# Performance work log

Measured on AMD Instinct MI355X. Metric: run time of the kernel, lower is better.

## Reference

```python
import jax, jax.numpy as jnp
import numpy as np
import math

# Config (mirrors KoopmanConfig)
B = 4096          # batch
C = 128           # context_dim
D = 32            # latent_dim
K = 8             # num_experts
R = 8             # low_rank
NSEG = 3
STEPS = [8, 8, 8] # steps_per_segment, sums to HORIZON
HORIZON = 24
DT = 0.1
DECAY_TARGET = 0.7
DECAY_SCALE = 1.0
SIGMA_MAX = 1.0
MAX_FROB = 3.0
TEMP = 2.0        # gate_temperature_start (stage 1)
EPS = 1e-6


def expm_fixed(M):
    """Matrix exponential via scaling-and-squaring + Taylor (Horner).
    Valid because ||M*dt|| is small (A Frobenius-clamped to 3, Q diag <= 1, dt=0.1).
    Fully differentiable and batched over leading dims."""
    SQ = 6       # scale by 2^-6 -> norm ~0.01
    ORDER = 14
    A = M / (2.0 ** SQ)
    n = M.shape[-1]
    I = jnp.eye(n, dtype=M.dtype)
    Rm = I
    for k in range(ORDER, 0, -1):
        Rm = I + (A @ Rm) / k
    for _ in range(SQ):
        Rm = Rm @ Rm
    return Rm


def setup_inputs() -> dict:
    key = jax.random.key(0)
    ks = jax.random.split(key, 10)
    def init(k, shape, fan_in):
        return jax.random.normal(k, shape, jnp.float32) / np.float32(np.sqrt(fan_in))
    return {
        "context": jax.random.normal(ks[0], (B, C), jnp.float32),
        "z0": jax.random.normal(ks[1], (B, D), jnp.float32),
        # per-segment stacked Linear params (torch Linear: y = x @ W + b)
        "S_W": init(ks[2], (NSEG, C, K * D * D), C),
        "S_b": jnp.zeros((NSEG, K * D * D), jnp.float32),
        "L_W": init(ks[3], (NSEG, C, K * D * R), C),
        "L_b": jnp.zeros((NSEG, K * D * R), jnp.float32),
        "G_W": init(ks[4], (NSEG, C, K), C),
        "G_b": jnp.zeros((NSEG, K), jnp.float32),
        "Sig_W": init(ks[5], (NSEG, C, D), C),
        "Sig_b": jnp.zeros((NSEG, D), jnp.float32),
    }


def reference(context, z0, S_W, S_b, L_W, L_b, G_W, G_b, Sig_W, Sig_b):
    b = context.shape[0]
    mu = jnp.float32(-math.log(DECAY_TARGET) / (DT * HORIZON) * DECAY_SCALE)
    I = jnp.eye(D, dtype=context.dtype)
    z = z0
    cov = jnp.zeros((b, D, D), context.dtype)
    states_all, covs_all = [], []
    for s in range(NSEG):
        # SegmentExpertGenerator
        raw_S = (context @ S_W[s] + S_b[s]).reshape(b, K, D, D)
        skew = raw_S - jnp.swapaxes(raw_S, -1, -2)
        raw_L = (context @ L_W[s] + L_b[s]).reshape(b, K, D, R)
        LLT = jnp.einsum('bkdr,bker->bkde', raw_L, raw_L)
        A_experts = skew - LLT - mu * I                      # [b,K,D,D]
        logits = context @ G_W[s] + G_b[s]
        w = jax.nn.softmax(logits / max(TEMP, EPS), axis=-1)  # [b,K]
        A = jnp.einsum('bk,bkde->bde', w, A_experts)
        # clamp_frobenius
        frob = jnp.linalg.norm(A.reshape(b, -1), axis=-1)
        scale = jnp.where(frob > MAX_FROB, MAX_FROB / (frob + EPS), jnp.float32(1.0))
        A = A * scale[:, None, None]
        # SigmaGenerator: diagonal Sigma -> Q = Sigma Sigma^T = diag(diag^2)
        diag = jnp.minimum(jax.nn.softplus(context @ Sig_W[s] + Sig_b[s]), SIGMA_MAX)
        Q = (diag ** 2)[:, :, None] * I                      # [b,D,D]
        # Van Loan discretization: expm([[A, Q], [0, -A^T]] * dt)
        top = jnp.concatenate([A, Q], axis=-1)
        bot = jnp.concatenate([jnp.zeros_like(Q), -jnp.swapaxes(A, -1, -2)], axis=-1)
        M = jnp.concatenate([top, bot], axis=-2)             # [b,2D,2D]
        E = expm_fixed(M * DT)
        Phi = E[..., :D, :D]
        Qd = Phi @ E[..., :D, D:]
        Qd = 0.5 * (Qd + jnp.swapaxes(Qd, -1, -2))
        PhiT = jnp.swapaxes(Phi, -1, -2)
        def step(carry, _):
            zc, cc = carry
            zc = jnp.einsum('bij,bj->bi', Phi, zc)
            cc = Phi @ cc @ PhiT + Qd
            cc = 0.5 * (cc + jnp.swapaxes(cc, -1, -2))
            return (zc, cc), (zc, cc)
        (z, cov), (zs, cs) = jax.lax.scan(step, (z, cov), None, length=STEPS[s])
        states_all.append(jnp.swapaxes(zs, 0, 1))   # [b,steps,D]
        covs_all.append(jnp.swapaxes(cs, 0, 1))     # [b,steps,D,D]
    states = jnp.concatenate(states_all, axis=1)    # [b,HORIZON,D]
    covariances = jnp.concatenate(covs_all, axis=1) # [b,HORIZON,D,D]
    return states, covariances
```

## Files before the change

### kernel.cpp

```cpp
#include <hip/hip_runtime.h>
#include <math.h>


#define NSEGC 3
#define BSZ   4096
#define MUC   0.14861455999447191f
#define XSC   0.025f
#define XRS(r) (((r) & 7) << 2)

typedef unsigned short ushort_t;
typedef unsigned int uint_t;
typedef __attribute__((ext_vector_type(8))) short bf16x8;
typedef __attribute__((ext_vector_type(16))) float f32x16;

__device__ __forceinline__ void ld4(float d[4], const float* p) {
  const float4 v = *(const float4*)p; d[0]=v.x; d[1]=v.y; d[2]=v.z; d[3]=v.w;
}
__device__ __forceinline__ void st4(float* p, const float d[4]) {
  *(float4*)p = make_float4(d[0], d[1], d[2], d[3]);
}
__device__ __forceinline__ unsigned short bf_rne(float x) {
  unsigned b = __float_as_uint(x);
  unsigned r = b + 0x7FFFu + ((b >> 16) & 1u);
  return (unsigned short)(r >> 16);
}
__device__ __forceinline__ float bf2f(short v) {
  return __uint_as_float(((uint_t)(unsigned short)v) << 16);
}

__global__ __launch_bounds__(64) void kA(const float* __restrict__ ctx,
    const float* __restrict__ GW, const float* __restrict__ Gb,
    const float* __restrict__ SgW, const float* __restrict__ Sgb,
    float* __restrict__ Wsm, float* __restrict__ Q2) {
  const int b = blockIdx.x, s = blockIdx.y, l = threadIdx.x;
  __shared__ float c[128];
  c[l]      = ctx[(size_t)b*128 + l];
  c[l + 64] = ctx[(size_t)b*128 + 64 + l];
  __syncthreads();
  if (l < 8) {
    float acc = Gb[s*8 + l];
    #pragma unroll 4
    for (int q = 0; q < 128; ++q) acc += c[q] * GW[(size_t)(s*128 + q)*8 + l];
    float li = acc * 0.5f;
    float m = li;
    m = fmaxf(m, __shfl_xor(m, 1));
    m = fmaxf(m, __shfl_xor(m, 2));
    m = fmaxf(m, __shfl_xor(m, 4));
    float e = expf(li - m);
    float sum = e;
    sum += __shfl_xor(sum, 1);
    sum += __shfl_xor(sum, 2);
    sum += __shfl_xor(sum, 4);
    Wsm[((size_t)s*BSZ + b)*8 + l] = e / sum;
  } else if (l < 40) {
    const int d = l - 8;
    float acc = Sgb[s*32 + d];
    #pragma unroll 4
    for (int q = 0; q < 128; ++q) acc += c[q] * SgW[(size_t)(s*128 + q)*32 + d];
    float sp = fmaxf(acc, 0.f) + log1pf(expf(-fabsf(acc)));
    float dg = fminf(sp, 1.0f);
    Q2[((size_t)s*BSZ + b)*32 + d] = dg * dg;
  }
}

__global__ __launch_bounds__(256) void kT(const float* __restrict__ SW,
                                          float* __restrict__ SWT) {
  __shared__ float mt[1056];
  const int kc = blockIdx.x, s = blockIdx.y, t = threadIdx.x;
  const int k = kc >> 7, c = kc & 127;
  const float* src = SW + ((size_t)(s*128 + c))*8192 + (size_t)k*1024;
  float* dst = SWT + ((size_t)s*1024 + kc)*1024;
  for (int i = t; i < 1024; i += 256) mt[(i >> 5)*33 + (i & 31)] = src[i];
  __syncthreads();
  for (int i = t; i < 1024; i += 256) dst[i] = mt[(i & 31)*33 + (i >> 5)];
}

__global__ __launch_bounds__(256) void kCvtB(const float* __restrict__ SW,
    const float* __restrict__ SWT, const float* __restrict__ Sb,
    ushort_t* __restrict__ Bh, ushort_t* __restrict__ Bl) {
  const int s = blockIdx.y, t = threadIdx.x;
  const int n0 = blockIdx.x * 16;
  const int tn = t & 15, tck = t >> 4;
  const int n = n0 + tn;
  const int nT = (n & 31)*32 + (n >> 5);
  ushort_t* bh = Bh + (size_t)s*1114112;
  ushort_t* bl = Bl + (size_t)s*1114112;
  for (int kc0 = 0; kc0 < 1088; kc0 += 16) {
    const int kc = kc0 + tck;
    float v = 0.f;
    if (kc < 1024) {
      const int k = kc >> 7, c = kc & 127;
      v = SW[((size_t)(s*128 + c))*8192 + (size_t)k*1024 + n]
        - SWT[((size_t)s*1024 + kc)*1024 + n];
    } else if (kc < 1032) {
      const int k2 = kc - 1024;
      const float* base = Sb + (size_t)s*8192 + (size_t)k2*1024;
      v = base[n] - base[nT];
    }
    const unsigned short h = bf_rne(v);
    bh[(size_t)n*1088 + kc] = h;
    bl[(size_t)n*1088 + kc] = bf_rne(v - __uint_as_float(((unsigned)h) << 16));
  }
}

__global__ __launch_bounds__(256) void kCvtX(const float* __restrict__ ctx,
    ushort_t* __restrict__ Xh, ushort_t* __restrict__ Xl) {
  const int idx = blockIdx.x*256 + threadIdx.x;
  const float v = ctx[idx];
  const unsigned short h = bf_rne(v);
  Xh[idx] = h;
  Xl[idx] = bf_rne(v - __uint_as_float(((unsigned)h) << 16));
}

__global__ __launch_bounds__(256) void kCvtL(const float* __restrict__ LW,
    ushort_t* __restrict__ Lh, ushort_t* __restrict__ Ll) {
  __shared__ float tile[32][33];
  const int nb = blockIdx.x * 32, cb = blockIdx.y * 32, s = blockIdx.z;
  const int tx = threadIdx.x & 31, ty = threadIdx.x >> 5;
  for (int r = ty; r < 32; r += 8)
    tile[r][tx] = LW[((size_t)(s*128 + cb + r))*2048 + nb + tx];
  __syncthreads();
  for (int r = ty; r < 32; r += 8) {
    const float v = tile[tx][r];
    const unsigned short h = bf_rne(v);
    const size_t o = ((size_t)s*2048 + nb + r)*128 + cb + tx;
    Lh[o] = h;
    Ll[o] = bf_rne(v - __uint_as_float(((unsigned)h) << 16));
  }
}

__global__ __launch_bounds__(256) void kCvtA(const float* __restrict__ ctx,
    const float* __restrict__ Wsm, ushort_t* __restrict__ Ah,
    ushort_t* __restrict__ Al, int s) {
  __shared__ float cs[128];
  __shared__ float wwv[8];
  const int b = blockIdx.x, t = threadIdx.x;
  if (t < 128) cs[t] = ctx[(size_t)b*128 + t];
  else if (t < 136) wwv[t - 128] = Wsm[((size_t)s*BSZ + b)*8 + (t - 128)];
  __syncthreads();
  for (int kc = t; kc < 1088; kc += 256) {
    float v = 0.f;
    if (kc < 1024) v = wwv[kc >> 7] * cs[kc & 127];
    else if (kc < 1032) v = wwv[kc - 1024];
    const unsigned short h = bf_rne(v);
    const float hf = __uint_as_float(((unsigned)h) << 16);
    Ah[(size_t)b*1088 + kc] = h;
    Al[(size_t)b*1088 + kc] = bf_rne(v - hf);
  }
}

__global__ __launch_bounds__(256) void kB3(const ushort_t* __restrict__ Ah,
    const ushort_t* __restrict__ Al, const ushort_t* __restrict__ Bh,
    const ushort_t* __restrict__ Bl, float* __restrict__ ASseg) {
  __shared__ ushort_t sArr[2][2][8192];
  const int t = threadIdx.x;
  const int l = t & 63, w = t >> 6;
  const int hh = l >> 5, lane31 = l & 31;
  const int nb = blockIdx.x * 128, bb = blockIdx.y * 128;
  const int wr0 = (w & 1) * 64, wc0 = (w >> 1) * 64;

  const ushort_t* APT[3] = {Ah, Ah, Al};
  const ushort_t* BPT[3] = {Bh, Bl, Bh};

  f32x16 acc[2][2];
  #pragma unroll
  for (int a = 0; a < 2; ++a)
    #pragma unroll
    for (int bq = 0; bq < 2; ++bq)
      #pragma unroll
      for (int e = 0; e < 16; ++e) acc[a][bq][e] = 0.f;

  #define STAGE(buf, it) do {                                                  \
    const int p_ = (it) / 17, ks_ = (it) - p_*17;                              \
    const ushort_t* As_ = APT[p_];                                             \
    const ushort_t* Bs_ = BPT[p_];                                             \
    _Pragma("unroll")                                                          \
    for (int i_ = 0; i_ < 4; ++i_) {                                           \
      const int gidx_ = i_*256 + t;                                            \
      const int r_ = gidx_ >> 3, g_ = gidx_ & 7;                               \
      const int gs_ = g_ ^ (r_ & 7);                                           \
      const ushort_t* srcA_ = As_ + (size_t)(bb + r_)*1088 + ks_*64 + gs_*8;   \
      const ushort_t* srcB_ = Bs_ + (size_t)(nb + r_)*1088 + ks_*64 + gs_*8;   \
      __builtin_amdgcn_global_load_lds(                                        \
        (const __attribute__((address_space(1))) unsigned int*)srcA_,          \
        (__attribute__((address_space(3))) unsigned int*)&sArr[buf][0][(i_*256 + w*64)*8], \
        16, 0, 0);                                                             \
      __builtin_amdgcn_global_load_lds(                                        \
        (const __attribute__((address_space(1))) unsigned int*)srcB_,          \
        (__attribute__((address_space(3))) unsigned int*)&sArr[buf][1][(i_*256 + w*64)*8], \
        16, 0, 0);                                                             \
    }                                                                          \
  } while (0)

  STAGE(0, 0);
  int cur = 0;
  #pragma unroll 1
  for (int it = 0; it < 51; ++it) {
    __syncthreads();
    if (it + 1 < 51) STAGE(cur ^ 1, it + 1);
    const ushort_t* lA = &sArr[cur][0][0];
    const ushort_t* lB = &sArr[cur][1][0];
    #pragma unroll
    for (int kc = 0; kc < 4; ++kc) {
      bf16x8 af[2], bfr[2];
      #pragma unroll
      for (int rt = 0; rt < 2; ++rt) {
        const int row = wr0 + rt*32 + lane31;
        const int slot = (kc*2 + hh) ^ (row & 7);
        af[rt] = *(const bf16x8*)&lA[row*64 + slot*8];
      }
      #pragma unroll
      for (int ct = 0; ct < 2; ++ct) {
        const int row = wc0 + ct*32 + lane31;
        const int slot = (kc*2 + hh) ^ (row & 7);
        bfr[ct] = *(const bf16x8*)&lB[row*64 + slot*8];
      }
      #pragma unroll
      for (int rt = 0; rt < 2; ++rt)
        #pragma unroll
        for (int ct = 0; ct < 2; ++ct)
          acc[rt][ct] = __builtin_amdgcn_mfma_f32_32x32x16_bf16(
              af[rt], bfr[ct], acc[rt][ct], 0, 0, 0);
    }
    cur ^= 1;
  }
  #undef STAGE

  #pragma unroll
  for (int rt = 0; rt < 2; ++rt)
    #pragma unroll
    for (int ct = 0; ct < 2; ++ct) {
      float* o = ASseg + ((size_t)(bb + wr0 + rt*32))*1024 + nb + wc0 + ct*32 + lane31;
      #pragma unroll
      for (int reg = 0; reg < 16; ++reg) {
        const int row = (reg & 3) + 8*(reg >> 2) + 4*hh;
        o[(size_t)row*1024] = acc[rt][ct][reg];
      }
    }
}

__global__ __launch_bounds__(256) void kL3(const ushort_t* __restrict__ Xh,
    const ushort_t* __restrict__ Xl, const ushort_t* __restrict__ Lh,
    const ushort_t* __restrict__ Ll, const float* __restrict__ Lb,
    const float* __restrict__ Wsm, float* __restrict__ lt, int s) {
  __shared__ ushort_t sArr[2][2][8192];
  __shared__ float sqw[128][8];
  const int t = threadIdx.x;
  const int l = t & 63, w = t >> 6;
  const int hh = l >> 5, lane31 = l & 31;
  const int nb = blockIdx.x * 128, bb = blockIdx.y * 128;
  const int wr0 = (w & 1) * 64, wc0 = (w >> 1) * 64;
  for (int i = t; i < 1024; i += 256)
    sqw[i >> 3][i & 7] = sqrtf(Wsm[((size_t)s*BSZ + bb + (i >> 3))*8 + (i & 7)]);

  const ushort_t* APT[3] = {Xh, Xh, Xl};
  const ushort_t* BPT[3] = {Lh + (size_t)s*262144, Ll + (size_t)s*262144,
                            Lh + (size_t)s*262144};

  f32x16 acc[2][2];
  #pragma unroll
  for (int a = 0; a < 2; ++a)
    #pragma unroll
    for (int bq = 0; bq < 2; ++bq)
      #pragma unroll
      for (int e = 0; e < 16; ++e) acc[a][bq][e] = 0.f;

  #define STAGEL(buf, it) do {                                                 \
    const int p_ = (it) >> 1, ks_ = (it) & 1;                                  \
    const ushort_t* As_ = APT[p_];                                             \
    const ushort_t* Bs_ = BPT[p_];                                             \
    _Pragma("unroll")                                                          \
    for (int i_ = 0; i_ < 4; ++i_) {                                           \
      const int gidx_ = i_*256 + t;                                            \
      const int r_ = gidx_ >> 3, g_ = gidx_ & 7;                               \
      const int gs_ = g_ ^ (r_ & 7);                                           \
      const ushort_t* srcA_ = As_ + (size_t)(bb + r_)*128 + ks_*64 + gs_*8;    \
      const ushort_t* srcB_ = Bs_ + (size_t)(nb + r_)*128 + ks_*64 + gs_*8;    \
      __builtin_amdgcn_global_load_lds(                                        \
        (const __attribute__((address_space(1))) unsigned int*)srcA_,          \
        (__attribute__((address_space(3))) unsigned int*)&sArr[buf][0][(i_*256 + w*64)*8], \
        16, 0, 0);                                                             \
      __builtin_amdgcn_global_load_lds(                                        \
        (const __attribute__((address_space(1))) unsigned int*)srcB_,          \
        (__attribute__((address_space(3))) unsigned int*)&sArr[buf][1][(i_*256 + w*64)*8], \
        16, 0, 0);                                                             \
    }                                                                          \
  } while (0)

  STAGEL(0, 0);
  int cur = 0;
  #pragma unroll 1
  for (int it = 0; it < 6; ++it) {
    __syncthreads();
    if (it + 1 < 6) STAGEL(cur ^ 1, it + 1);
    const ushort_t* lA = &sArr[cur][0][0];
    const ushort_t* lB = &sArr[cur][1][0];
    #pragma unroll
    for (int kc = 0; kc < 4; ++kc) {
      bf16x8 af[2], bfr[2];
      #pragma unroll
      for (int rt = 0; rt < 2; ++rt) {
        const int row = wr0 + rt*32 + lane31;
        const int slot = (kc*2 + hh) ^ (row & 7);
        af[rt] = *(const bf16x8*)&lA[row*64 + slot*8];
      }
      #pragma unroll
      for (int ct = 0; ct < 2; ++ct) {
        const int row = wc0 + ct*32 + lane31;
        const int slot = (kc*2 + hh) ^ (row & 7);
        bfr[ct] = *(const bf16x8*)&lB[row*64 + slot*8];
      }
      #pragma unroll
      for (int rt = 0; rt < 2; ++rt)
        #pragma unroll
        for (int ct = 0; ct < 2; ++ct)
          acc[rt][ct] = __builtin_amdgcn_mfma_f32_32x32x16_bf16(
              af[rt], bfr[ct], acc[rt][ct], 0, 0, 0);
    }
    cur ^= 1;
  }
  #undef STAGEL

  #pragma unroll
  for (int rt = 0; rt < 2; ++rt)
    #pragma unroll
    for (int ct = 0; ct < 2; ++ct) {
      const int n = nb + wc0 + ct*32 + lane31;
      const float lb = Lb[(size_t)s*2048 + n];
      const int kidx = n >> 8;
      const int ltcol = (kidx << 8) + ((n & 7) << 5) + ((n >> 3) & 31);
      #pragma unroll
      for (int reg = 0; reg < 16; ++reg) {
        const int lrow = wr0 + rt*32 + (reg & 3) + 8*(reg >> 2) + 4*hh;
        lt[(size_t)(bb + lrow)*2048 + ltcol] =
            (acc[rt][ct][reg] + lb) * sqw[lrow][kidx];
      }
    }
}

__global__ __launch_bounds__(128) void kLLT(const float* __restrict__ LT,
                                            float* __restrict__ AS, int s) {
  __shared__ float L4[4][64][32];
  const int t = threadIdx.x;
  const int bbase = blockIdx.x * 4;
  {
    float* l4f = &L4[0][0][0];
    const float* src = LT + (size_t)bbase * 2048;
    for (int i = t*4; i < 8192; i += 512)
      *(float4*)&l4f[i] = *(const float4*)&src[i];
  }
  __syncthreads();
  const int b = t >> 5, u = t & 31;
  const int i0 = (u >> 2) * 4, j0 = (u & 3) * 8;
  float acc[4][8] = {};
  #pragma unroll 8
  for (int kr = 0; kr < 64; ++kr) {
    float pa[4], pb[8];
    ld4(pa, &L4[b][kr][i0]);
    ld4(pb, &L4[b][kr][j0]); ld4(pb + 4, &L4[b][kr][j0 + 4]);
    #pragma unroll
    for (int ii = 0; ii < 4; ++ii)
      #pragma unroll
      for (int jj = 0; jj < 8; ++jj) acc[ii][jj] += pa[ii] * pb[jj];
  }
  float* dst = AS + ((size_t)s*BSZ + bbase + b)*1024;
  for (int ii = 0; ii < 4; ++ii) {
    float x[8];
    ld4(x, &dst[(i0+ii)*32 + j0]); ld4(x + 4, &dst[(i0+ii)*32 + j0 + 4]);
    #pragma unroll
    for (int jj = 0; jj < 8; ++jj) x[jj] -= acc[ii][jj];
    st4(&dst[(i0+ii)*32 + j0], x); st4(&dst[(i0+ii)*32 + j0 + 4], &x[4]);
  }
}

struct Frag { bf16x8 h0, l0, h1, l1; };

__device__ __forceinline__ void cvt8(const float x[8], bf16x8& hi, bf16x8& lo) {
  uint_t h[4], l[4];
  #pragma unroll
  for (int p = 0; p < 4; ++p) {
    const uint_t b0 = __float_as_uint(x[2*p]);
    const uint_t b1 = __float_as_uint(x[2*p + 1]);
    h[p] = __builtin_amdgcn_perm(b1, b0, 0x07060302u);
    const float l0f = x[2*p]     - __uint_as_float(b0 & 0xFFFF0000u);
    const float l1f = x[2*p + 1] - __uint_as_float(b1 & 0xFFFF0000u);
    l[p] = __builtin_amdgcn_perm(__float_as_uint(l1f), __float_as_uint(l0f),
                                 0x07060302u);
  }
  hi = __builtin_bit_cast(bf16x8, make_uint4(h[0], h[1], h[2], h[3]));
  lo = __builtin_bit_cast(bf16x8, make_uint4(l[0], l[1], l[2], l[3]));
}
__device__ __forceinline__ void rd_row8(const float* M, int r, int kb, float o[8]) {
  const float* p = M + r*32;
  ld4(o,     p + ((kb)     ^ XRS(r)));
  ld4(o + 4, p + ((kb + 4) ^ XRS(r)));
}
__device__ __forceinline__ void rd_col8(const float* M, int c, int kb, float o[8]) {
  #pragma unroll
  for (int e = 0; e < 8; ++e) o[e] = M[(kb + e)*32 + (c ^ XRS(kb + e))];
}
__device__ __forceinline__ void mkfrag_row(const float* M, int r, int hoff, Frag& f) {
  float t0[8], t1[8];
  rd_row8(M, r, hoff, t0);
  rd_row8(M, r, 16 + hoff, t1);
  cvt8(t0, f.h0, f.l0);
  cvt8(t1, f.h1, f.l1);
}
__device__ __forceinline__ void mkfrag_col(const float* M, int c, int hoff, Frag& f) {
  float t0[8], t1[8];
  rd_col8(M, c, hoff, t0);
  rd_col8(M, c, 16 + hoff, t1);
  cvt8(t0, f.h0, f.l0);
  cvt8(t1, f.h1, f.l1);
}
__device__ __forceinline__ f32x16 mmacc(const Frag& A, const Frag& B, f32x16 acc) {
  acc = __builtin_amdgcn_mfma_f32_32x32x16_bf16(A.h0, B.h0, acc, 0, 0, 0);
  acc = __builtin_amdgcn_mfma_f32_32x32x16_bf16(A.h0, B.l0, acc, 0, 0, 0);
  acc = __builtin_amdgcn_mfma_f32_32x32x16_bf16(A.l0, B.h0, acc, 0, 0, 0);
  acc = __builtin_amdgcn_mfma_f32_32x32x16_bf16(A.h1, B.h1, acc, 0, 0, 0);
  acc = __builtin_amdgcn_mfma_f32_32x32x16_bf16(A.h1, B.l1, acc, 0, 0, 0);
  acc = __builtin_amdgcn_mfma_f32_32x32x16_bf16(A.l1, B.h1, acc, 0, 0, 0);
  return acc;
}
__device__ __forceinline__ f32x16 zero16() {
  f32x16 z = {0.f,0.f,0.f,0.f,0.f,0.f,0.f,0.f,0.f,0.f,0.f,0.f,0.f,0.f,0.f,0.f};
  return z;
}
__device__ __forceinline__ void st_T(float* M, int j, int ho4, const float v[16]) {
  float* p = M + j*32;
  #pragma unroll
  for (int m = 0; m < 4; ++m) st4(p + ((8*m + ho4) ^ XRS(j)), v + 4*m);
}
__device__ __forceinline__ void ld16_T(const float* M, int j, int ho4, float o[16]) {
  const float* p = M + j*32;
  #pragma unroll
  for (int m = 0; m < 4; ++m) ld4(o + 4*m, p + ((8*m + ho4) ^ XRS(j)));
}

__global__ __launch_bounds__(64, 3) void kC12(const float* __restrict__ AS,
    const float* __restrict__ Q2, const float* __restrict__ z0,
    float* __restrict__ out) {
  __shared__ float S11[1024];
  __shared__ float S12[1024];
  __shared__ float S22[1024];
  __shared__ float zarr[32], qds[32];
  const int b = blockIdx.x, t = threadIdx.x;
  const int j = t & 31, hh = t >> 5;
  const int hoff = hh * 8, ho4 = hh * 4;

  if (t < 32) zarr[t] = z0[(size_t)b*32 + t];
  float covreg[16];
  #pragma unroll
  for (int r = 0; r < 16; ++r) covreg[r] = 0.f;
  __syncthreads();

  float* covout = out + 3145728 + (size_t)b*24576;
  float* stout  = out + (size_t)b*768;

  for (int s = 0; s < NSEGC; ++s) {
    if (t < 32) qds[t] = Q2[((size_t)s*BSZ + b)*32 + t] * XSC;
    const float* asb = AS + ((size_t)s*BSZ + b)*1024;
    float av[16];
    #pragma unroll
    for (int m = 0; m < 4; ++m) ld4(av + 4*m, &asb[j*32 + 16*hh + 4*m]);
    #pragma unroll
    for (int i = 0; i < 16; ++i) if (16*hh + i == j) av[i] -= MUC;
    float ssq = 0.f;
    #pragma unroll
    for (int i = 0; i < 16; ++i) ssq += av[i]*av[i];
    #pragma unroll
    for (int off = 1; off < 64; off <<= 1) ssq += __shfl_xor(ssq, off);
    const float frob = sqrtf(ssq);
    const float sc = (frob > 3.0f ? 3.0f / (frob + 1e-6f) : 1.0f) * XSC;
    #pragma unroll
    for (int i = 0; i < 16; ++i) av[i] *= sc;
    __syncthreads();
    #pragma unroll
    for (int m = 0; m < 4; ++m)
      st4(&S12[j*32 + ((16*hh + 4*m) ^ XRS(j))], av + 4*m);
    __syncthreads();
    Frag aA, aT;
    mkfrag_row(S12, j, hoff, aA);
    mkfrag_col(S12, j, hoff, aT);
    __syncthreads();
    #pragma unroll
    for (int m = 0; m < 4; ++m) {
      float id[4], zo[4] = {0.f, 0.f, 0.f, 0.f};
      #pragma unroll
      for (int e = 0; e < 4; ++e) id[e] = (16*hh + 4*m + e == j) ? 1.f : 0.f;
      st4(&S11[j*32 + ((16*hh + 4*m) ^ XRS(j))], id);
      st4(&S22[j*32 + ((16*hh + 4*m) ^ XRS(j))], id);
      st4(&S12[j*32 + ((16*hh + 4*m) ^ XRS(j))], zo);
    }
    __syncthreads();
    float qv[16];
    #pragma unroll
    for (int r = 0; r < 16; ++r) qv[r] = qds[(r&3) + 8*(r>>2) + ho4];

    for (int k = 4; k >= 1; --k) {
      const float rk = 1.0f / (float)k;
      Frag Bf;
      float Xs[16];
      mkfrag_row(S11, j, hoff, Bf);
      f32x16 X = mmacc(aA, Bf, zero16());
      #pragma unroll
      for (int r = 0; r < 16; ++r) {
        const int row = (r&3) + 8*(r>>2) + ho4;
        Xs[r] = X[r]*rk + (row == j ? 1.f : 0.f);
      }
      st_T(S11, j, ho4, Xs);
      mkfrag_row(S12, j, hoff, Bf);
      X = mmacc(aA, Bf, zero16());
      float rv[16];
      ld16_T(S22, j, ho4, rv);
      #pragma unroll
      for (int r = 0; r < 16; ++r) Xs[r] = (X[r] + qv[r]*rv[r]) * rk;
      st_T(S12, j, ho4, Xs);
      mkfrag_row(S22, j, hoff, Bf);
      X = mmacc(aT, Bf, zero16());
      #pragma unroll
      for (int r = 0; r < 16; ++r) {
        const int row = (r&3) + 8*(r>>2) + ho4;
        Xs[r] = (row == j ? 1.f : 0.f) - X[r]*rk;
      }
      st_T(S22, j, ho4, Xs);
    }
    __syncthreads();

    {
      Frag Ac, Br;
      float Xs[16];
      mkfrag_col(S11, j, hoff, Ac);
      mkfrag_row(S11, j, hoff, Br);
      f32x16 X1 = mmacc(Ac, Br, zero16());
      #pragma unroll
      for (int r = 0; r < 16; ++r) Xs[r] = X1[r];
      st_T(S11, j, ho4, Xs);
      Frag B12; mkfrag_row(S12, j, hoff, B12);
      f32x16 X2 = mmacc(Ac, B12, zero16());
      Frag A12; mkfrag_col(S12, j, hoff, A12);
      Frag B22; mkfrag_row(S22, j, hoff, B22);
      X2 = mmacc(A12, B22, X2);
      #pragma unroll
      for (int r = 0; r < 16; ++r) Xs[r] = X2[r];
      st_T(S12, j, ho4, Xs);
      Frag A22; mkfrag_col(S22, j, hoff, A22);
      f32x16 X3 = mmacc(A22, B22, zero16());
      #pragma unroll
      for (int r = 0; r < 16; ++r) Xs[r] = X3[r];
      st_T(S22, j, ho4, Xs);
    }
    __syncthreads();
    {
      Frag Ac, Br;
      float Xs[16];
      mkfrag_col(S11, j, hoff, Ac);
      mkfrag_row(S11, j, hoff, Br);
      f32x16 X1 = mmacc(Ac, Br, zero16());
      Frag B12; mkfrag_row(S12, j, hoff, B12);
      f32x16 X2 = mmacc(Ac, B12, zero16());
      Frag A12; mkfrag_col(S12, j, hoff, A12);
      Frag B22; mkfrag_row(S22, j, hoff, B22);
      X2 = mmacc(A12, B22, X2);
      #pragma unroll
      for (int r = 0; r < 16; ++r) Xs[r] = X1[r];
      st_T(S11, j, ho4, Xs);
      #pragma unroll
      for (int r = 0; r < 16; ++r) Xs[r] = X2[r];
      st_T(S12, j, ho4, Xs);
    }
    __syncthreads();

    Frag PhiF;
    mkfrag_col(S11, j, hoff, PhiF);
    {
      Frag B12; mkfrag_row(S12, j, hoff, B12);
      f32x16 Xq = mmacc(PhiF, B12, zero16());
      float Xs[16];
      #pragma unroll
      for (int r = 0; r < 16; ++r) Xs[r] = Xq[r];
      st_T(S22, j, ho4, Xs);
      __syncthreads();
      float sym[16];
      #pragma unroll
      for (int r = 0; r < 16; ++r) {
        const int row = (r&3) + 8*(r>>2) + ho4;
        const float tv = S22[row*32 + (j ^ XRS(row))];
        sym[r] = 0.5f * (Xs[r] + tv);
      }
      __syncthreads();
      st_T(S22, j, ho4, sym);
    }
    __syncthreads();

    st_T(S12, j, ho4, covreg);
    __syncthreads();

    for (int tt = 0; tt < 8; ++tt) {
      Frag Bcov; mkfrag_row(S12, j, hoff, Bcov);
      f32x16 G = mmacc(PhiF, Bcov, zero16());
      float Gs[16];
      #pragma unroll
      for (int r = 0; r < 16; ++r) Gs[r] = G[r];
      st_T(S11, j, ho4, Gs);
      Frag AG; mkfrag_col(S11, j, hoff, AG);
      f32x16 C = mmacc(AG, PhiF, zero16());
      float qdv[16], Cs[16];
      ld16_T(S22, j, ho4, qdv);
      #pragma unroll
      for (int r = 0; r < 16; ++r) Cs[r] = C[r] + qdv[r];
      float zp = 0.f;
      #pragma unroll
      for (int e = 0; e < 8; ++e) {
        zp += (bf2f(PhiF.h0[e]) + bf2f(PhiF.l0[e])) * zarr[hoff + e];
        zp += (bf2f(PhiF.h1[e]) + bf2f(PhiF.l1[e])) * zarr[16 + hoff + e];
      }
      zp += __shfl_xor(zp, 32);
      st_T(S12, j, ho4, Cs);
      #pragma unroll
      for (int r = 0; r < 16; ++r) covreg[r] = Cs[r];
      float* cb = covout + (size_t)(s*8 + tt)*1024;
      #pragma unroll
      for (int r = 0; r < 16; ++r)
        cb[((r&3) + 8*(r>>2) + ho4)*32 + j] = Cs[r];
      if (t < 32) {
        zarr[t] = zp;
        stout[(s*8 + tt)*32 + t] = zp;
      }
      __syncthreads();
    }
  }
}

extern "C" void kernel_launch(void* const* d_in, const int* in_sizes, int n_in,
                              void* d_out, int out_size, void* d_ws, size_t ws_size,
                              hipStream_t stream) {
  const float* ctx  = (const float*)d_in[0];
  const float* z0   = (const float*)d_in[1];
  const float* S_W  = (const float*)d_in[2];
  const float* S_b  = (const float*)d_in[3];
  const float* L_W  = (const float*)d_in[4];
  const float* L_b  = (const float*)d_in[5];
  const float* G_W  = (const float*)d_in[6];
  const float* G_b  = (const float*)d_in[7];
  const float* Sg_W = (const float*)d_in[8];
  const float* Sg_b = (const float*)d_in[9];
  float* out = (float*)d_out;
  float* ws  = (float*)d_ws;

  float* w_   = ws;
  float* q2   = ws + 98304;
  float* as_  = ws + 1015808;
  float* swt  = ws + 1015808;
  ushort_t* panAh  = (ushort_t*)(ws + 13598720);
  ushort_t* panAl  = panAh + 4456448;
  ushort_t* panBh3 = panAl + 4456448;
  ushort_t* panBl3 = panBh3 + 3342336;
  float* lt = ws + 13598720;
  ushort_t* cxh = (ushort_t*)(ws + 21987328);
  ushort_t* cxl = cxh + 524288;
  ushort_t* lwh = cxl + 524288;
  ushort_t* lwl = lwh + 786432;

  kA   <<<dim3(4096, 3), 64,  0, stream>>>(ctx, G_W, G_b, Sg_W, Sg_b, w_, q2);
  kCvtX<<<dim3(2048),    256, 0, stream>>>(ctx, cxh, cxl);
  kCvtL<<<dim3(64, 4, 3),256, 0, stream>>>(L_W, lwh, lwl);
  kT   <<<dim3(1024, 3), 256, 0, stream>>>(S_W, swt);
  kCvtB<<<dim3(64, 3),   256, 0, stream>>>(S_W, swt, S_b, panBh3, panBl3);
  for (int s = 0; s < 3; ++s) {
    kCvtA<<<dim3(4096), 256, 0, stream>>>(ctx, w_, panAh, panAl, s);
    kB3  <<<dim3(8, 32), 256, 0, stream>>>(panAh, panAl,
                                           panBh3 + (size_t)s*1114112,
                                           panBl3 + (size_t)s*1114112,
                                           as_ + (size_t)s*4194304);
  }
  for (int s = 0; s < 3; ++s) {
    kL3 <<<dim3(16, 32), 256, 0, stream>>>(cxh, cxl, lwh, lwl, L_b, w_, lt, s);
    kLLT<<<dim3(1024),   128, 0, stream>>>(lt, as_, s);
  }
  kC12<<<dim3(4096),    64, 0, stream>>>(as_, q2, z0, out);
}
```

Before: 626.0 us.

## Fuse low-rank LLT product into per-segment propagation kernel via split-bf16 MFMA

After: 545.0 us. -12.9%, faster.

```diff
diff --git a/kernel.cpp b/kernel.cpp
--- a/kernel.cpp
+++ b/kernel.cpp
@@ -239,10 +239,11 @@
     }
 }
 
-__global__ __launch_bounds__(256) void kL3(const ushort_t* __restrict__ Xh,
+__global__ __launch_bounds__(256) void kL4(const ushort_t* __restrict__ Xh,
     const ushort_t* __restrict__ Xl, const ushort_t* __restrict__ Lh,
     const ushort_t* __restrict__ Ll, const float* __restrict__ Lb,
-    const float* __restrict__ Wsm, float* __restrict__ lt, int s) {
+    const float* __restrict__ Wsm, ushort_t* __restrict__ LTh,
+    ushort_t* __restrict__ LTl, int s) {
   __shared__ ushort_t sArr[2][2][8192];
   __shared__ float sqw[128][8];
   const int t = threadIdx.x;
@@ -328,49 +329,18 @@
       const int n = nb + wc0 + ct*32 + lane31;
       const float lb = Lb[(size_t)s*2048 + n];
       const int kidx = n >> 8;
-      const int ltcol = (kidx << 8) + ((n & 7) << 5) + ((n >> 3) & 31);
+      const int d = (n >> 3) & 31, r = n & 7;
+      const size_t coloff = (size_t)d*64 + kidx*8 + r;
       #pragma unroll
       for (int reg = 0; reg < 16; ++reg) {
         const int lrow = wr0 + rt*32 + (reg & 3) + 8*(reg >> 2) + 4*hh;
-        lt[(size_t)(bb + lrow)*2048 + ltcol] =
-            (acc[rt][ct][reg] + lb) * sqw[lrow][kidx];
+        const float v = (acc[rt][ct][reg] + lb) * sqw[lrow][kidx];
+        const unsigned short h = bf_rne(v);
+        const size_t o = (size_t)(bb + lrow)*2048 + coloff;
+        LTh[o] = h;
+        LTl[o] = bf_rne(v - __uint_as_float(((unsigned)h) << 16));
       }
     }
-}
-
-__global__ __launch_bounds__(128) void kLLT(const float* __restrict__ LT,
-                                            float* __restrict__ AS, int s) {
-  __shared__ float L4[4][64][32];
-  const int t = threadIdx.x;
-  const int bbase = blockIdx.x * 4;
-  {
-    float* l4f = &L4[0][0][0];
-    const float* src = LT + (size_t)bbase * 2048;
-    for (int i = t*4; i < 8192; i += 512)
-      *(float4*)&l4f[i] = *(const float4*)&src[i];
-  }
-  __syncthreads();
-  const int b = t >> 5, u = t & 31;
-  const int i0 = (u >> 2) * 4, j0 = (u & 3) * 8;
-  float acc[4][8] = {};
-  #pragma unroll 8
-  for (int kr = 0; kr < 64; ++kr) {
-    float pa[4], pb[8];
-    ld4(pa, &L4[b][kr][i0]);
-    ld4(pb, &L4[b][kr][j0]); ld4(pb + 4, &L4[b][kr][j0 + 4]);
-    #pragma unroll
-    for (int ii = 0; ii < 4; ++ii)
-      #pragma unroll
-      for (int jj = 0; jj < 8; ++jj) acc[ii][jj] += pa[ii] * pb[jj];
-  }
-  float* dst = AS + ((size_t)s*BSZ + bbase + b)*1024;
-  for (int ii = 0; ii < 4; ++ii) {
-    float x[8];
-    ld4(x, &dst[(i0+ii)*32 + j0]); ld4(x + 4, &dst[(i0+ii)*32 + j0 + 4]);
-    #pragma unroll
-    for (int jj = 0; jj < 8; ++jj) x[jj] -= acc[ii][jj];
-    st4(&dst[(i0+ii)*32 + j0], x); st4(&dst[(i0+ii)*32 + j0 + 4], &x[4]);
-  }
 }
 
 struct Frag { bf16x8 h0, l0, h1, l1; };
@@ -437,9 +407,10 @@
   for (int m = 0; m < 4; ++m) ld4(o + 4*m, p + ((8*m + ho4) ^ XRS(j)));
 }
 
-__global__ __launch_bounds__(64, 3) void kC12(const float* __restrict__ AS,
+__global__ __launch_bounds__(64, 3) void kC13(const float* __restrict__ AS,
     const float* __restrict__ Q2, const float* __restrict__ z0,
-    float* __restrict__ out) {
+    const ushort_t* __restrict__ LTh, const ushort_t* __restrict__ LTl,
+    float* __restrict__ out, int s) {
   __shared__ float S11[1024];
   __shared__ float S12[1024];
   __shared__ float S22[1024];
@@ -448,187 +419,208 @@
   const int j = t & 31, hh = t >> 5;
   const int hoff = hh * 8, ho4 = hh * 4;
 
-  if (t < 32) zarr[t] = z0[(size_t)b*32 + t];
-  float covreg[16];
-  #pragma unroll
-  for (int r = 0; r < 16; ++r) covreg[r] = 0.f;
-  __syncthreads();
-
   float* covout = out + 3145728 + (size_t)b*24576;
   float* stout  = out + (size_t)b*768;
 
-  for (int s = 0; s < NSEGC; ++s) {
-    if (t < 32) qds[t] = Q2[((size_t)s*BSZ + b)*32 + t] * XSC;
-    const float* asb = AS + ((size_t)s*BSZ + b)*1024;
-    float av[16];
-    #pragma unroll
-    for (int m = 0; m < 4; ++m) ld4(av + 4*m, &asb[j*32 + 16*hh + 4*m]);
-    #pragma unroll
-    for (int i = 0; i < 16; ++i) if (16*hh + i == j) av[i] -= MUC;
-    float ssq = 0.f;
-    #pragma unroll
-    for (int i = 0; i < 16; ++i) ssq += av[i]*av[i];
-    #pragma unroll
-    for (int off = 1; off < 64; off <<= 1) ssq += __shfl_xor(ssq, off);
-    const float frob = sqrtf(ssq);
-    const float sc = (frob > 3.0f ? 3.0f / (frob + 1e-6f) : 1.0f) * XSC;
-    #pragma unroll
-    for (int i = 0; i < 16; ++i) av[i] *= sc;
+  if (t < 32) {
+    zarr[t] = (s == 0) ? z0[(size_t)b*32 + t] : stout[(8*s - 1)*32 + t];
+    qds[t] = Q2[((size_t)s*BSZ + b)*32 + t] * XSC;
+  }
+  float covreg[16];
+  if (s == 0) {
+    #pragma unroll
+    for (int r = 0; r < 16; ++r) covreg[r] = 0.f;
+  } else {
+    const float* cbp = covout + (size_t)(8*s - 1)*1024;
+    #pragma unroll
+    for (int r = 0; r < 16; ++r)
+      covreg[r] = cbp[((r&3) + 8*(r>>2) + ho4)*32 + j];
+  }
+
+  f32x16 llt = zero16();
+  {
+    const ushort_t* ph = LTh + (size_t)b*2048 + j*64 + hoff;
+    const ushort_t* pl = LTl + (size_t)b*2048 + j*64 + hoff;
+    Frag FA, FB;
+    FA.h0 = *(const bf16x8*)&ph[0];  FA.l0 = *(const bf16x8*)&pl[0];
+    FA.h1 = *(const bf16x8*)&ph[16]; FA.l1 = *(const bf16x8*)&pl[16];
+    FB.h0 = *(const bf16x8*)&ph[32]; FB.l0 = *(const bf16x8*)&pl[32];
+    FB.h1 = *(const bf16x8*)&ph[48]; FB.l1 = *(const bf16x8*)&pl[48];
+    llt = mmacc(FA, FA, llt);
+    llt = mmacc(FB, FB, llt);
+  }
+
+  const float* asb = AS + ((size_t)s*BSZ + b)*1024;
+  float av[16];
+  #pragma unroll
+  for (int m = 0; m < 4; ++m) ld4(av + 4*m, &asb[j*32 + 8*m + ho4]);
+  #pragma unroll
+  for (int r = 0; r < 16; ++r) {
+    av[r] -= llt[r];
+    const int col = (r & 3) + 8*(r >> 2) + ho4;
+    if (col == j) av[r] -= MUC;
+  }
+  float ssq = 0.f;
+  #pragma unroll
+  for (int r = 0; r < 16; ++r) ssq += av[r]*av[r];
+  #pragma unroll
+  for (int off = 1; off < 64; off <<= 1) ssq += __shfl_xor(ssq, off);
+  const float frob = sqrtf(ssq);
+  const float sc = (frob > 3.0f ? 3.0f / (frob + 1e-6f) : 1.0f) * XSC;
+  #pragma unroll
+  for (int r = 0; r < 16; ++r) av[r] *= sc;
+  __syncthreads();
+  #pragma unroll
+  for (int m = 0; m < 4; ++m)
+    st4(&S12[j*32 + ((8*m + ho4) ^ XRS(j))], av + 4*m);
+  __syncthreads();
+  Frag aA, aT;
+  mkfrag_row(S12, j, hoff, aA);
+  mkfrag_col(S12, j, hoff, aT);
+  __syncthreads();
+  #pragma unroll
+  for (int m = 0; m < 4; ++m) {
+    float id[4], zo[4] = {0.f, 0.f, 0.f, 0.f};
+    #pragma unroll
+    for (int e = 0; e < 4; ++e) id[e] = (16*hh + 4*m + e == j) ? 1.f : 0.f;
+    st4(&S11[j*32 + ((16*hh + 4*m) ^ XRS(j))], id);
+    st4(&S22[j*32 + ((16*hh + 4*m) ^ XRS(j))], id);
+    st4(&S12[j*32 + ((16*hh + 4*m) ^ XRS(j))], zo);
+  }
+  __syncthreads();
+  float qv[16];
+  #pragma unroll
+  for (int r = 0; r < 16; ++r) qv[r] = qds[(r&3) + 8*(r>>2) + ho4];
+
+  for (int k = 4; k >= 1; --k) {
+    const float rk = 1.0f / (float)k;
+    Frag Bf;
+    float Xs[16];
+    mkfrag_row(S11, j, hoff, Bf);
+    f32x16 X = mmacc(aA, Bf, zero16());
+    #pragma unroll
+    for (int r = 0; r < 16; ++r) {
+      const int row = (r&3) + 8*(r>>2) + ho4;
+      Xs[r] = X[r]*rk + (row == j ? 1.f : 0.f);
+    }
+    st_T(S11, j, ho4, Xs);
+    mkfrag_row(S12, j, hoff, Bf);
+    X = mmacc(aA, Bf, zero16());
+    float rv[16];
+    ld16_T(S22, j, ho4, rv);
+    #pragma unroll
+    for (int r = 0; r < 16; ++r) Xs[r] = (X[r] + qv[r]*rv[r]) * rk;
+    st_T(S12, j, ho4, Xs);
+    mkfrag_row(S22, j, hoff, Bf);
+    X = mmacc(aT, Bf, zero16());
+    #pragma unroll
+    for (int r = 0; r < 16; ++r) {
+      const int row = (r&3) + 8*(r>>2) + ho4;
+      Xs[r] = (row == j ? 1.f : 0.f) - X[r]*rk;
+    }
+    st_T(S22, j, ho4, Xs);
+  }
+  __syncthreads();
+
+  {
+    Frag Ac, Br;
+    float Xs[16];
+    mkfrag_col(S11, j, hoff, Ac);
+    mkfrag_row(S11, j, hoff, Br);
+    f32x16 X1 = mmacc(Ac, Br, zero16());
+    #pragma unroll
+    for (int r = 0; r < 16; ++r) Xs[r] = X1[r];
+    st_T(S11, j, ho4, Xs);
+    Frag B12; mkfrag_row(S12, j, hoff, B12);
+    f32x16 X2 = mmacc(Ac, B12, zero16());
+    Frag A12; mkfrag_col(S12, j, hoff, A12);
+    Frag B22; mkfrag_row(S22, j, hoff, B22);
+    X2 = mmacc(A12, B22, X2);
+    #pragma unroll
+    for (int r = 0; r < 16; ++r) Xs[r] = X2[r];
+    st_T(S12, j, ho4, Xs);
+    Frag A22; mkfrag_col(S22, j, hoff, A22);
+    f32x16 X3 = mmacc(A22, B22, zero16());
+    #pragma unroll
+    for (int r = 0; r < 16; ++r) Xs[r] = X3[r];
+    st_T(S22, j, ho4, Xs);
+  }
+  __syncthreads();
+  {
+    Frag Ac, Br;
+    float Xs[16];
+    mkfrag_col(S11, j, hoff, Ac);
+    mkfrag_row(S11, j, hoff, Br);
+    f32x16 X1 = mmacc(Ac, Br, zero16());
+    Frag B12; mkfrag_row(S12, j, hoff, B12);
+    f32x16 X2 = mmacc(Ac, B12, zero16());
+    Frag A12; mkfrag_col(S12, j, hoff, A12);
+    Frag B22; mkfrag_row(S22, j, hoff, B22);
+    X2 = mmacc(A12, B22, X2);
+    #pragma unroll
+    for (int r = 0; r < 16; ++r) Xs[r] = X1[r];
+    st_T(S11, j, ho4, Xs);
+    #pragma unroll
+    for (int r = 0; r < 16; ++r) Xs[r] = X2[r];
+    st_T(S12, j, ho4, Xs);
+  }
+  __syncthreads();
+
+  Frag PhiF;
+  mkfrag_col(S11, j, hoff, PhiF);
+  {
+    Frag B12; mkfrag_row(S12, j, hoff, B12);
+    f32x16 Xq = mmacc(PhiF, B12, zero16());
+    float Xs[16];
+    #pragma unroll
+    for (int r = 0; r < 16; ++r) Xs[r] = Xq[r];
+    st_T(S22, j, ho4, Xs);
     __syncthreads();
-    #pragma unroll
-    for (int m = 0; m < 4; ++m)
-      st4(&S12[j*32 + ((16*hh + 4*m) ^ XRS(j))], av + 4*m);
+    float sym[16];
+    #pragma unroll
+    for (int r = 0; r < 16; ++r) {
+      const int row = (r&3) + 8*(r>>2) + ho4;
+      const float tv = S22[row*32 + (j ^ XRS(row))];
+      sym[r] = 0.5f * (Xs[r] + tv);
+    }
     __syncthreads();
-    Frag aA, aT;
-    mkfrag_row(S12, j, hoff, aA);
-    mkfrag_col(S12, j, hoff, aT);
+    st_T(S22, j, ho4, sym);
+  }
+  __syncthreads();
+
+  st_T(S12, j, ho4, covreg);
+  __syncthreads();
+
+  for (int tt = 0; tt < 8; ++tt) {
+    Frag Bcov; mkfrag_row(S12, j, hoff, Bcov);
+    f32x16 G = mmacc(PhiF, Bcov, zero16());
+    float Gs[16];
+    #pragma unroll
+    for (int r = 0; r < 16; ++r) Gs[r] = G[r];
+    st_T(S11, j, ho4, Gs);
+    Frag AG; mkfrag_col(S11, j, hoff, AG);
+    f32x16 C = mmacc(AG, PhiF, zero16());
+    float qdv[16], Cs[16];
+    ld16_T(S22, j, ho4, qdv);
+    #pragma unroll
+    for (int r = 0; r < 16; ++r) Cs[r] = C[r] + qdv[r];
+    float zp = 0.f;
+    #pragma unroll
+    for (int e = 0; e < 8; ++e) {
+      zp += (bf2f(PhiF.h0[e]) + bf2f(PhiF.l0[e])) * zarr[hoff + e];
+      zp += (bf2f(PhiF.h1[e]) + bf2f(PhiF.l1[e])) * zarr[16 + hoff + e];
+    }
+    zp += __shfl_xor(zp, 32);
+    st_T(S12, j, ho4, Cs);
+    float* cb = covout + (size_t)(s*8 + tt)*1024;
+    #pragma unroll
+    for (int r = 0; r < 16; ++r)
+      cb[((r&3) + 8*(r>>2) + ho4)*32 + j] = Cs[r];
+    if (t < 32) {
+      zarr[t] = zp;
+      stout[(s*8 + tt)*32 + t] = zp;
+    }
     __syncthreads();
-    #pragma unroll
-    for (int m = 0; m < 4; ++m) {
-      float id[4], zo[4] = {0.f, 0.f, 0.f, 0.f};
-      #pragma unroll
-      for (int e = 0; e < 4; ++e) id[e] = (16*hh + 4*m + e == j) ? 1.f : 0.f;
-      st4(&S11[j*32 + ((16*hh + 4*m) ^ XRS(j))], id);
-      st4(&S22[j*32 + ((16*hh + 4*m) ^ XRS(j))], id);
-      st4(&S12[j*32 + ((16*hh + 4*m) ^ XRS(j))], zo);
-    }
-    __syncthreads();
-    float qv[16];
-    #pragma unroll
-    for (int r = 0; r < 16; ++r) qv[r] = qds[(r&3) + 8*(r>>2) + ho4];
-
-    for (int k = 4; k >= 1; --k) {
-      const float rk = 1.0f / (float)k;
-      Frag Bf;
-      float Xs[16];
-      mkfrag_row(S11, j, hoff, Bf);
-      f32x16 X = mmacc(aA, Bf, zero16());
-      #pragma unroll
-      for (int r = 0; r < 16; ++r) {
-        const int row = (r&3) + 8*(r>>2) + ho4;
-        Xs[r] = X[r]*rk + (row == j ? 1.f : 0.f);
-      }
-      st_T(S11, j, ho4, Xs);
-      mkfrag_row(S12, j, hoff, Bf);
-      X = mmacc(aA, Bf, zero16());
-      float rv[16];
-      ld16_T(S22, j, ho4, rv);
-      #pragma unroll
-      for (int r = 0; r < 16; ++r) Xs[r] = (X[r] + qv[r]*rv[r]) * rk;
-      st_T(S12, j, ho4, Xs);
-      mkfrag_row(S22, j, hoff, Bf);
-      X = mmacc(aT, Bf, zero16());
-      #pragma unroll
-      for (int r = 0; r < 16; ++r) {
-        const int row = (r&3) + 8*(r>>2) + ho4;
-        Xs[r] = (row == j ? 1.f : 0.f) - X[r]*rk;
-      }
-      st_T(S22, j, ho4, Xs);
-    }
-    __syncthreads();
-
-    {
-      Frag Ac, Br;
-      float Xs[16];
-      mkfrag_col(S11, j, hoff, Ac);
-      mkfrag_row(S11, j, hoff, Br);
-      f32x16 X1 = mmacc(Ac, Br, zero16());
-      #pragma unroll
-      for (int r = 0; r < 16; ++r) Xs[r] = X1[r];
-      st_T(S11, j, ho4, Xs);
-      Frag B12; mkfrag_row(S12, j, hoff, B12);
-      f32x16 X2 = mmacc(Ac, B12, zero16());
-      Frag A12; mkfrag_col(S12, j, hoff, A12);
-      Frag B22; mkfrag_row(S22, j, hoff, B22);
-      X2 = mmacc(A12, B22, X2);
-      #pragma unroll
-      for (int r = 0; r < 16; ++r) Xs[r] = X2[r];
-      st_T(S12, j, ho4, Xs);
-      Frag A22; mkfrag_col(S22, j, hoff, A22);
-      f32x16 X3 = mmacc(A22, B22, zero16());
-      #pragma unroll
-      for (int r = 0; r < 16; ++r) Xs[r] = X3[r];
-      st_T(S22, j, ho4, Xs);
-    }
-    __syncthreads();
-    {
-      Frag Ac, Br;
-      float Xs[16];
-      mkfrag_col(S11, j, hoff, Ac);
-      mkfrag_row(S11, j, hoff, Br);
-      f32x16 X1 = mmacc(Ac, Br, zero16());
-      Frag B12; mkfrag_row(S12, j, hoff, B12);
-      f32x16 X2 = mmacc(Ac, B12, zero16());
-      Frag A12; mkfrag_col(S12, j, hoff, A12);
-      Frag B22; mkfrag_row(S22, j, hoff, B22);
-      X2 = mmacc(A12, B22, X2);
-      #pragma unroll
-      for (int r = 0; r < 16; ++r) Xs[r] = X1[r];
-      st_T(S11, j, ho4, Xs);
-      #pragma unroll
-      for (int r = 0; r < 16; ++r) Xs[r] = X2[r];
-      st_T(S12, j, ho4, Xs);
-    }
-    __syncthreads();
-
-    Frag PhiF;
-    mkfrag_col(S11, j, hoff, PhiF);
-    {
-      Frag B12; mkfrag_row(S12, j, hoff, B12);
-      f32x16 Xq = mmacc(PhiF, B12, zero16());
-      float Xs[16];
-      #pragma unroll
-      for (int r = 0; r < 16; ++r) Xs[r] = Xq[r];
-      st_T(S22, j, ho4, Xs);
-      __syncthreads();
-      float sym[16];
-      #pragma unroll
-      for (int r = 0; r < 16; ++r) {
-        const int row = (r&3) + 8*(r>>2) + ho4;
-        const float tv = S22[row*32 + (j ^ XRS(row))];
-        sym[r] = 0.5f * (Xs[r] + tv);
-      }
-      __syncthreads();
-      st_T(S22, j, ho4, sym);
-    }
-    __syncthreads();
-
-    st_T(S12, j, ho4, covreg);
-    __syncthreads();
-
-    for (int tt = 0; tt < 8; ++tt) {
-      Frag Bcov; mkfrag_row(S12, j, hoff, Bcov);
-      f32x16 G = mmacc(PhiF, Bcov, zero16());
-      float Gs[16];
-      #pragma unroll
-      for (int r = 0; r < 16; ++r) Gs[r] = G[r];
-      st_T(S11, j, ho4, Gs);
-      Frag AG; mkfrag_col(S11, j, hoff, AG);
-      f32x16 C = mmacc(AG, PhiF, zero16());
-      float qdv[16], Cs[16];
-      ld16_T(S22, j, ho4, qdv);
-      #pragma unroll
-      for (int r = 0; r < 16; ++r) Cs[r] = C[r] + qdv[r];
-      float zp = 0.f;
-      #pragma unroll
-      for (int e = 0; e < 8; ++e) {
-        zp += (bf2f(PhiF.h0[e]) + bf2f(PhiF.l0[e])) * zarr[hoff + e];
-        zp += (bf2f(PhiF.h1[e]) + bf2f(PhiF.l1[e])) * zarr[16 + hoff + e];
-      }
-      zp += __shfl_xor(zp, 32);
-      st_T(S12, j, ho4, Cs);
-      #pragma unroll
-      for (int r = 0; r < 16; ++r) covreg[r] = Cs[r];
-      float* cb = covout + (size_t)(s*8 + tt)*1024;
-      #pragma unroll
-      for (int r = 0; r < 16; ++r)
-        cb[((r&3) + 8*(r>>2) + ho4)*32 + j] = Cs[r];
-      if (t < 32) {
-        zarr[t] = zp;
-        stout[(s*8 + tt)*32 + t] = zp;
-      }
-      __syncthreads();
-    }
   }
 }
 
@@ -656,7 +648,8 @@
   ushort_t* panAl  = panAh + 4456448;
   ushort_t* panBh3 = panAl + 4456448;
   ushort_t* panBl3 = panBh3 + 3342336;
-  float* lt = ws + 13598720;
+  ushort_t* LTh = (ushort_t*)(ws + 13598720);
+  ushort_t* LTl = LTh + 8388608;
   ushort_t* cxh = (ushort_t*)(ws + 21987328);
   ushort_t* cxl = cxh + 524288;
   ushort_t* lwh = cxl + 524288;
@@ -675,8 +668,8 @@
                                            as_ + (size_t)s*4194304);
   }
   for (int s = 0; s < 3; ++s) {
-    kL3 <<<dim3(16, 32), 256, 0, stream>>>(cxh, cxl, lwh, lwl, L_b, w_, lt, s);
-    kLLT<<<dim3(1024),   128, 0, stream>>>(lt, as_, s);
-  }
-  kC12<<<dim3(4096),    64, 0, stream>>>(as_, q2, z0, out);
-}
+    kL4 <<<dim3(16, 32), 256, 0, stream>>>(cxh, cxl, lwh, lwl, L_b, w_,
+                                           LTh, LTl, s);
+    kC13<<<dim3(4096),   64,  0, stream>>>(as_, q2, z0, LTh, LTl, out, s);
+  }
+}
```
